# Optimization experiments

Hardware: AMD Instinct MI355X
Metric: run time of the kernel (lower is better)

## Reference

```python
import jax, jax.numpy as jnp
import numpy as np

C = 256        # in_channels == depth
HEADS = 8
K = 251        # kernel_size == attended axis length
DH = C // HEADS  # 32
EPS = 1e-5


def _bn(x, g, b, axes, ch_axis):
    # training-mode batchnorm: batch statistics, biased variance
    m = jnp.mean(x, axes, keepdims=True)
    v = jnp.var(x, axes, keepdims=True)
    shape = [1] * x.ndim
    shape[ch_axis] = -1
    return (x - m) / jnp.sqrt(v + EPS) * g.reshape(shape) + b.reshape(shape)


def _axial_cross(x, y, wk, wq, wv, gk, bk, gq, bq, gkq, bkq, glog, blog, rel):
    B, _, H, W = x.shape  # [B, C, H, W], height_dim=False -> attend over W
    # permute(0,2,1,3) then fold freq axis into batch: [B*H, C, W]
    xb = x.transpose(0, 2, 1, 3).reshape(B * H, C, W)
    yb = y.transpose(0, 2, 1, 3).reshape(B * H, C, W)
    # 1x1 conv1d == channel-mixing einsum, then BN over (batch, length)
    k = _bn(jnp.einsum('oc,bcl->bol', wk, xb), gk, bk, (0, 2), 1)
    q = _bn(jnp.einsum('oc,bcl->bol', wq, yb), gq, bq, (0, 2), 1)
    v = _bn(jnp.einsum('oc,bcl->bol', wv, xb), gkq, bkq, (0, 2), 1)  # original uses kq_bn on v
    kqv = jnp.concatenate([k, q, v], axis=1).reshape(B * H, HEADS, DH * 2, W)
    k = kqv[:, :, : DH // 2]          # [b, h, dh/2, W]
    q = kqv[:, :, DH // 2: DH]        # [b, h, dh/2, W]
    v = kqv[:, :, DH:]                # [b, h, dh,   W]
    # relative position encodings gathered by distance
    ki = jnp.arange(K)
    dist = (ki[None, :] - ki[:, None] + K - 1).reshape(-1)
    rel_e = rel[:, dist].reshape(DH * 2, K, K)
    q_enc = rel_e[: DH // 2]
    k_enc = rel_e[DH // 2: DH]
    v_enc = rel_e[DH:]
    qk = jnp.einsum('bhdx,bhdy->bhxy', q, k)
    qr = jnp.einsum('bhdx,dxy->bhxy', q, q_enc)
    kr = jnp.einsum('bhdx,dxy->bhxy', k, k_enc).transpose(0, 1, 3, 2)
    logits = jnp.concatenate([qk, qr, kr], axis=1)  # [b, 3*h, W, W]
    logits = _bn(logits, glog, blog, (0, 2, 3), 1)  # BatchNorm2d on 3*h channels
    logits = logits.reshape(B * H, 3, HEADS, W, W).sum(axis=1)
    weights = jax.nn.softmax(logits, axis=3)
    attn = jnp.einsum('bhxy,bhdy->bhdx', weights, v)        # [b, h, dh, W]
    attn_enc = jnp.einsum('bhxy,dxy->bhdx', weights, v_enc)  # [b, h, dh, W]
    attn_out = jnp.concatenate([attn, attn_enc], axis=-1)    # cat along length axis (as in original)
    attn_out = attn_out.reshape(B * H, C * 2, W)
    out = attn_out.reshape(B, H, C, 2, W).sum(axis=3)        # [B, H, C, W]
    return out.transpose(0, 2, 1, 3)                          # [B, C, H, W]


def setup_inputs() -> dict:
    key = jax.random.key(0)
    ks = jax.random.split(key, 6)
    B, H, W = 2, 15, 251
    sc = 0.05
    return {
        'x': jax.random.normal(ks[0], (B, C, H, W), jnp.float32),
        'y': jax.random.normal(ks[1], (B, C, H, W), jnp.float32),
        'wk': jax.random.normal(ks[2], (C // 2, C), jnp.float32) * sc,
        'wq': jax.random.normal(ks[3], (C // 2, C), jnp.float32) * sc,
        'wv': jax.random.normal(ks[4], (C, C), jnp.float32) * sc,
        'gk': jnp.ones((C // 2,), jnp.float32), 'bk': jnp.zeros((C // 2,), jnp.float32),
        'gq': jnp.ones((C // 2,), jnp.float32), 'bq': jnp.zeros((C // 2,), jnp.float32),
        'gkq': jnp.ones((C,), jnp.float32), 'bkq': jnp.zeros((C,), jnp.float32),
        'glog': jnp.ones((HEADS * 3,), jnp.float32), 'blog': jnp.zeros((HEADS * 3,), jnp.float32),
        'rel': jax.random.normal(ks[5], (DH * 2, 2 * K - 1), jnp.float32),
    }


def reference(x, y, wk, wq, wv, gk, bk, gq, bq, gkq, bkq, glog, blog, rel):
    return _axial_cross(x, y, wk, wq, wv, gk, bk, gq, bq, gkq, bkq, glog, blog, rel)
```

## Files before the change

### kernel.cpp

```cpp
#include <hip/hip_runtime.h>
#include <hip/hip_bf16.h>
#include <cstdint>

#define WPOS 251
#define NBB  30
#define NCH  512
#define RELP 501
#define NEPS 1e-5f

typedef _Float16 half2_t __attribute__((ext_vector_type(2)));
typedef _Float16 half8_t __attribute__((ext_vector_type(8)));
typedef float f32x16_t __attribute__((ext_vector_type(16)));

#if defined(__has_builtin)
#if __has_builtin(__builtin_amdgcn_fdot2)
#define FDOT2(a, b, c) __builtin_amdgcn_fdot2((a), (b), (c), false)
#endif
#endif
#ifndef FDOT2
#define FDOT2(a, b, c) ((float)(a)[0] * (float)(b)[0] + (float)(a)[1] * (float)(b)[1] + (c))
#endif

static constexpr size_t SZ_Z     = (size_t)NBB * NCH * WPOS;
static constexpr size_t OFF_Z    = 0;
static constexpr size_t OFF_VH   = OFF_Z + SZ_Z;
static constexpr size_t SZ_VH    = (size_t)NBB * 8 * 128 * 32;
static constexpr size_t OFF_RETC = OFF_VH + SZ_VH;
static constexpr size_t OFF_VETP = OFF_RETC + (size_t)RELP * 16;
static constexpr size_t OFF_P1Q  = OFF_VETP + (size_t)256 * 32;
static constexpr size_t OFF_P1K  = OFF_P1Q + (size_t)16 * 502;
static constexpr size_t OFF_P2Q  = OFF_P1K + (size_t)16 * 502;
static constexpr size_t OFF_P2K  = OFF_P2Q + (size_t)256 * 502;
static constexpr size_t OFF_LPP  = OFF_P2K + (size_t)256 * 502;
static constexpr size_t OFF_CPS  = OFF_LPP + (size_t)960 * 548;
static constexpr size_t OFF_CPS2 = OFF_CPS + (size_t)240 * 512;
static constexpr size_t OFF_CS   = OFF_CPS2 + (size_t)240 * 512;
static constexpr size_t OFF_CS2  = OFF_CS + 512;
static constexpr size_t OFF_LPF  = OFF_CS2 + 512;

static __device__ __forceinline__ unsigned packh2(float a, float b) {
  half2_t t;
  t[0] = (_Float16)a;
  t[1] = (_Float16)b;
  return __builtin_bit_cast(unsigned, t);
}
static __device__ __forceinline__ half2_t ash2(unsigned u) {
  return __builtin_bit_cast(half2_t, u);
}

__global__ __launch_bounds__(256) void k_pre(
    const float* __restrict__ rel, unsigned* __restrict__ retc, unsigned* __restrict__ vetp,
    float* __restrict__ p1q, float* __restrict__ p1k,
    float* __restrict__ p2q, float* __restrict__ p2k) {
  int blk = blockIdx.x;
  if (blk < 64) {
    int idx = blk * 256 + threadIdx.x;
    if (idx < RELP * 16) {
      int p = idx >> 4, j = idx & 15;
      float lo, hi;
      if (j < 8) {
        lo = rel[(size_t)(2 * j) * RELP + p];
        hi = rel[(size_t)(2 * j + 1) * RELP + p];
      } else {
        int jj = j - 8;
        lo = rel[(size_t)(16 + 2 * jj) * RELP + (500 - p)];
        hi = rel[(size_t)(17 + 2 * jj) * RELP + (500 - p)];
      }
      retc[(size_t)p * 16 + j] = packh2(lo, hi);
    } else if (idx < RELP * 16 + 256 * 32) {
      int i2 = idx - RELP * 16;
      int t = i2 >> 5, ch = i2 & 31;
      float lo = (2 * t <= 500) ? rel[(size_t)(32 + ch) * RELP + 2 * t] : 0.f;
      float hi = (2 * t + 1 <= 500) ? rel[(size_t)(32 + ch) * RELP + 2 * t + 1] : 0.f;
      vetp[(size_t)t * 32 + ch] = packh2(lo, hi);
    }
    return;
  }
  int task = blk - 64;
  const float* ra;
  const float* rb = nullptr;
  float* outp;
  if (task < 16)        { ra = rel + (size_t)task * RELP; outp = p1q + (size_t)task * 502; }
  else if (task < 32)   { ra = rel + (size_t)task * RELP; outp = p1k + (size_t)(task - 16) * 502; }
  else if (task < 288)  { int pr = task - 32;
                          ra = rel + (size_t)(pr >> 4) * RELP;
                          rb = rel + (size_t)(pr & 15) * RELP;
                          outp = p2q + (size_t)pr * 502; }
  else                  { int pr = task - 288;
                          ra = rel + (size_t)(16 + (pr >> 4)) * RELP;
                          rb = rel + (size_t)(16 + (pr & 15)) * RELP;
                          outp = p2k + (size_t)pr * 502; }
  __shared__ float buf[256];
  int t = threadIdx.x;
  int i0 = 2 * t, i1 = 2 * t + 1;
  float a0 = (i0 < RELP) ? (rb ? ra[i0] * rb[i0] : ra[i0]) : 0.f;
  float a1 = (i1 < RELP) ? (rb ? ra[i1] * rb[i1] : ra[i1]) : 0.f;
  buf[t] = a0 + a1;
  __syncthreads();
#pragma unroll
  for (int off = 1; off < 256; off <<= 1) {
    float v = buf[t];
    float add = (t >= off) ? buf[t - off] : 0.f;
    __syncthreads();
    buf[t] = v + add;
    __syncthreads();
  }
  float ex = buf[t] - (a0 + a1);
  if (i0 <= RELP) outp[i0] = ex;
  if (i1 <= RELP) outp[i1] = ex + a0;
}

__global__ __launch_bounds__(256) void k_gemm(
    const float* __restrict__ x, const float* __restrict__ y,
    const float* __restrict__ wk, const float* __restrict__ wq,
    const float* __restrict__ wv, float* __restrict__ z,
    float* __restrict__ cps, float* __restrict__ cps2) {
  int l0 = blockIdx.x * 64;
  int o0 = blockIdx.y * 64;
  int bb = blockIdx.z;
  int b = bb / 15, hi = bb % 15;
  const float* src;
  const float* wmat;
  int orow0;
  if (o0 < 128)      { wmat = wk; orow0 = o0;       src = x; }
  else if (o0 < 256) { wmat = wq; orow0 = o0 - 128; src = y; }
  else               { wmat = wv; orow0 = o0 - 256; src = x; }

  __shared__ _Float16 Ah[64][68];
  __shared__ _Float16 Bh[64][68];

  int tid = threadIdx.x;
  int lane = tid & 63, wv4 = tid >> 6;
  int wo = wv4 >> 1, wl = wv4 & 1;
  int m = lane & 31, kh = lane >> 5;

  f32x16_t acc = {};

  int cA = tid & 63, ogA = tid >> 6;
  int lB = tid & 63, kgB = tid >> 6;
  int lglob = l0 + lB;
  bool lok = (lglob < WPOS);
  const float* xcol = src + (size_t)(((size_t)b * 256) * 15 + hi) * WPOS + lglob;

  for (int c0 = 0; c0 < 256; c0 += 64) {
#pragma unroll
    for (int i = 0; i < 16; ++i) {
      int o = ogA * 16 + i;
      Ah[o][cA] = (_Float16)wmat[(size_t)(orow0 + o) * 256 + c0 + cA];
    }
#pragma unroll
    for (int i = 0; i < 16; ++i) {
      int k = kgB * 16 + i;
      float v = lok ? xcol[(size_t)(c0 + k) * 15 * WPOS] : 0.f;
      Bh[k][lB] = (_Float16)v;
    }
    __syncthreads();
#pragma unroll
    for (int ks = 0; ks < 4; ++ks) {
      const _Float16* ap = &Ah[wo * 32 + m][ks * 16 + kh * 8];
      uint2 aLo = *(const uint2*)(ap);
      uint2 aHi = *(const uint2*)(ap + 4);
      uint4 au = {aLo.x, aLo.y, aHi.x, aHi.y};
      half8_t af = __builtin_bit_cast(half8_t, au);
      half8_t bf;
      int kb = ks * 16 + kh * 8;
      int bcol = wl * 32 + m;
#pragma unroll
      for (int e = 0; e < 8; ++e) bf[e] = Bh[kb + e][bcol];
      acc = __builtin_amdgcn_mfma_f32_32x32x16_f16(af, bf, acc, 0, 0, 0);
    }
    __syncthreads();
  }

  int n = lane & 31;
  int lout = l0 + wl * 32 + n;
  if (lout < WPOS) {
#pragma unroll
    for (int r = 0; r < 16; ++r) {
      int mrow = (r & 3) + 8 * (r >> 2) + 4 * kh;
      int o = o0 + wo * 32 + mrow;
      z[((size_t)bb * NCH + o) * WPOS + lout] = acc[r];
    }
  }

  int part = (blockIdx.x * 2 + wl) * NBB + bb;
#pragma unroll
  for (int r = 0; r < 16; ++r) {
    float s = acc[r];
    float s2 = s * s;
#pragma unroll
    for (int m2 = 1; m2 < 32; m2 <<= 1) {
      s  += __shfl_xor(s, m2, 64);
      s2 += __shfl_xor(s2, m2, 64);
    }
    if (n == 0) {
      int mrow = (r & 3) + 8 * (r >> 2) + 4 * kh;
      int o = o0 + wo * 32 + mrow;
      cps[(size_t)part * 512 + o] = s;
      cps2[(size_t)part * 512 + o] = s2;
    }
  }
}

__global__ __launch_bounds__(256) void k_cred(
    const float* __restrict__ cps, const float* __restrict__ cps2,
    float* __restrict__ csum, float* __restrict__ csum2) {
  int c = blockIdx.x * 16 + (threadIdx.x & 15);
  int grp = threadIdx.x >> 4;
  __shared__ float r1[256], r2[256];
  float s = 0.f, s2 = 0.f;
  for (int i = 0; i < 15; ++i) {
    int p = grp * 15 + i;
    s += cps[(size_t)p * 512 + c];
    s2 += cps2[(size_t)p * 512 + c];
  }
  r1[threadIdx.x] = s; r2[threadIdx.x] = s2;
  __syncthreads();
  for (int st = 128; st >= 16; st >>= 1) {
    if (threadIdx.x < st) {
      r1[threadIdx.x] += r1[threadIdx.x + st];
      r2[threadIdx.x] += r2[threadIdx.x + st];
    }
    __syncthreads();
  }
  if (threadIdx.x < 16) {
    csum[c] = r1[threadIdx.x];
    csum2[c] = r2[threadIdx.x];
  }
}

__device__ __forceinline__ float block_reduce(float v, float* red, int tid) {
  red[tid] = v; __syncthreads();
  for (int s = 128; s > 0; s >>= 1) {
    if (tid < s) red[tid] += red[tid + s];
    __syncthreads();
  }
  float r = red[0]; __syncthreads();
  return r;
}

__device__ __forceinline__ void chan_affine(
    int ch, const float* gk, const float* bk, const float* gq, const float* bq,
    const float* gkq, const float* bkq, const float* csum, const float* csum2,
    float& a, float& bout) {
  float g, bi;
  if (ch < 128)      { g = gk[ch];        bi = bk[ch]; }
  else if (ch < 256) { g = gq[ch - 128];  bi = bq[ch - 128]; }
  else               { g = gkq[ch - 256]; bi = bkq[ch - 256]; }
  float n = (float)(NBB * WPOS);
  float mean = csum[ch] / n;
  float var = csum2[ch] / n - mean * mean;
  a = g / sqrtf(var + NEPS);
  bout = bi - mean * a;
}

__global__ __launch_bounds__(256) void k_mid(
    const float* __restrict__ z,
    const float* __restrict__ gk, const float* __restrict__ bk,
    const float* __restrict__ gq, const float* __restrict__ bq,
    const float* __restrict__ gkq, const float* __restrict__ bkq,
    const float* __restrict__ csum, const float* __restrict__ csum2,
    unsigned* __restrict__ vh,
    const float* __restrict__ p1q, const float* __restrict__ p1k,
    const float* __restrict__ p2q, const float* __restrict__ p2k,
    float* __restrict__ lpp) {
  int blk = blockIdx.x;
  bool isV = (blk < 960);
  int sblk = isV ? blk : blk - 960;
  int bbh = sblk % 240, sub = sblk / 240;
  int bb = bbh >> 3, h = bbh & 7;
  int tid = threadIdx.x;

  __shared__ __align__(16) float pool[16 * 68 * 2];
  __shared__ float red[256];
  __shared__ float caL[32], cbL[32];
  __shared__ int pairLUT[136];

  if (tid < 32) {
    int ch = h * 64 + (isV ? 32 + tid : tid);
    chan_affine(ch, gk, bk, gq, bq, gkq, bkq, csum, csum2, caL[tid], cbL[tid]);
  } else if (tid >= 64 && tid < 200) {
    int i = tid - 64, rem = i, d = 0;
    while (rem >= 16 - d) { rem -= 16 - d; ++d; }
    pairLUT[i] = (d << 4) | (d + rem);
  }
  __syncthreads();

  if (isV) {
    float (*T)[65] = (float(*)[65])pool;
    int l0 = sub * 64;
    const float* zv = z + ((size_t)bb * NCH + h * 64 + 32) * WPOS;
    for (int i = tid; i < 32 * 64; i += 256) {
      int ch = i >> 6, l = i & 63;
      int gl = l0 + l;
      T[ch][l] = (gl < WPOS) ? (caL[ch] * zv[(size_t)ch * WPOS + gl] + cbL[ch]) : 0.f;
    }
    __syncthreads();
    int p0 = l0 >> 1;
    for (int i = tid; i < 32 * 32; i += 256) {
      int pl = i >> 5, ch = i & 31;
      int gp = p0 + pl;
      if (gp < 128)
        vh[((size_t)bbh * 128 + gp) * 32 + ch] = packh2(T[ch][2 * pl], T[ch][2 * pl + 1]);
    }
    return;
  }

  float (*qs)[68] = (float(*)[68])pool;
  float (*ks)[68] = (float(*)[68])(pool + 16 * 68);
  int x0 = sub * 64;
  const float* zb = z + ((size_t)bb * NCH + h * 64) * WPOS;
  for (int idx = tid; idx < 16 * 64; idx += 256) {
    int d = idx >> 6, xl = idx & 63;
    int xg = x0 + xl;
    float kv = 0.f, qv = 0.f;
    if (xg < WPOS) {
      kv = caL[d] * zb[(size_t)d * WPOS + xg] + cbL[d];
      qv = caL[16 + d] * zb[(size_t)(16 + d) * WPOS + xg] + cbL[16 + d];
    }
    ks[d][xl] = kv; qs[d][xl] = qv;
  }
  __syncthreads();
  float* outp = lpp + ((size_t)bbh * 4 + sub) * 548;
  if (tid < 16) {
    float s = 0.f;
    for (int xl = 0; xl < 64; ++xl) s += qs[tid][xl];
    outp[516 + tid] = s;
  } else if (tid < 32) {
    float s = 0.f;
    for (int xl = 0; xl < 64; ++xl) s += ks[tid - 16][xl];
    outp[532 + (tid - 16)] = s;
  }
  {
    int d = tid >> 4, d2 = tid & 15;
    float g1 = 0.f, g2 = 0.f;
    for (int xl = 0; xl < 64; ++xl) {
      g1 += qs[d][xl] * qs[d2][xl];
      g2 += ks[d][xl] * ks[d2][xl];
    }
    outp[tid] = g1;
    outp[256 + tid] = g2;
  }
  float v_sumqr = 0.f, v_sqqr = 0.f, v_sumkr = 0.f, v_sqkr = 0.f;
  {
    int xl = tid & 63, wv = tid >> 6;
    int xg = x0 + xl;
    if (xg < WPOS) {
      int ihi = 501 - xg, ilo = 250 - xg;
      for (int i = wv; i < 136; i += 4) {
        int pc = pairLUT[i];
        int d = pc >> 4, d2 = pc & 15;
        float wgt = (d == d2) ? 1.f : 2.f;
        const float* pq = p2q + (size_t)(d * 16 + d2) * 502;
        const float* pk = p2k + (size_t)(d * 16 + d2) * 502;
        v_sqqr += wgt * qs[d][xl] * qs[d2][xl] * (pq[ihi] - pq[ilo]);
        v_sqkr += wgt * ks[d][xl] * ks[d2][xl] * (pk[ihi] - pk[ilo]);
      }
      for (int d = wv; d < 16; d += 4) {
        v_sumqr += qs[d][xl] * (p1q[d * 502 + ihi] - p1q[d * 502 + ilo]);
        v_sumkr += ks[d][xl] * (p1k[d * 502 + ihi] - p1k[d * 502 + ilo]);
      }
    }
  }
  float r1 = block_reduce(v_sumqr, red, tid);
  float r2 = block_reduce(v_sqqr, red, tid);
  float r3 = block_reduce(v_sumkr, red, tid);
  float r4 = block_reduce(v_sqkr, red, tid);
  if (tid == 0) { outp[512] = r1; outp[513] = r2; outp[514] = r3; outp[515] = r4; }
}

__global__ __launch_bounds__(256) void k_lstats2(const float* __restrict__ lpp,
                                                 float* __restrict__ lp) {
  int bbh = blockIdx.x;
  int tid = threadIdx.x;
  __shared__ float red[256];
  __shared__ float qsums[16], ksums[16];
  const float* b0 = lpp + (size_t)bbh * 4 * 548;
  float qg = b0[tid] + b0[548 + tid] + b0[1096 + tid] + b0[1644 + tid];
  float kg = b0[256 + tid] + b0[804 + tid] + b0[1352 + tid] + b0[1900 + tid];
  if (tid < 16) {
    qsums[tid] = b0[516 + tid] + b0[1064 + tid] + b0[1612 + tid] + b0[2160 + tid];
    ksums[tid] = b0[532 + tid] + b0[1080 + tid] + b0[1628 + tid] + b0[2176 + tid];
  }
  float sqqk = block_reduce(qg * kg, red, tid);
  if (tid == 0) {
    float sum_qk = 0.f;
    for (int d = 0; d < 16; ++d) sum_qk += qsums[d] * ksums[d];
    float s1 = 0.f, s2 = 0.f, s3 = 0.f, s4 = 0.f;
    for (int c = 0; c < 4; ++c) {
      const float* bc = b0 + (size_t)c * 548;
      s1 += bc[512]; s2 += bc[513]; s3 += bc[514]; s4 += bc[515];
    }
    float* o = lp + (size_t)bbh * 6;
    o[0] = sum_qk; o[1] = sqqk;
    o[2] = s1; o[3] = s2; o[4] = s3; o[5] = s4;
  }
}

__global__ __launch_bounds__(256) void k_attn(
    const float* __restrict__ z,
    const float* __restrict__ gk, const float* __restrict__ bk,
    const float* __restrict__ gq, const float* __restrict__ bq,
    const float* __restrict__ gkq, const float* __restrict__ bkq,
    const float* __restrict__ csum, const float* __restrict__ csum2,
    const unsigned* __restrict__ vh,
    const unsigned* __restrict__ retc, const unsigned* __restrict__ vetp,
    const float* __restrict__ lp, const float* __restrict__ glog,
    float* __restrict__ out) {
  int blk = blockIdx.x;
  int bbh = blk % 240, tile = blk / 240;
  int bb = bbh >> 3, h = bbh & 7;
  int b = bb / 15, hi = bb % 15;
  int x0 = tile * 32;
  int nr = min(32, WPOS - x0);
  int tid = threadIdx.x;
  int lane = tid & 63, wvid = tid >> 6;

  const float LOG2E = 1.4426950408889634f;

  __shared__ __align__(16) unsigned Su[32 * 132];
  __shared__ __align__(16) unsigned winU[282 * 18];
  __shared__ __align__(16) unsigned uSh[256];
  __shared__ float affL[72];
  _Float16* S = (_Float16*)Su;
  unsigned* qsP = uSh;
  float* sred = (float*)uSh;
  float* Cred = (float*)winU;

  int pwin0 = 251 - x0 - nr;
  int nwin = 250 + nr;

  if (tid < 32) {
    int ch = h * 64 + tid;
    chan_affine(ch, gk, bk, gq, bq, gkq, bkq, csum, csum2, affL[tid], affL[32 + tid]);
  } else if (tid >= 64 && tid < 70) {
    int grp = (tid - 64) >> 1, off = (tid - 64) & 1;
    float s = 0.f;
    for (int bb2 = 0; bb2 < NBB; ++bb2)
      s += lp[(size_t)(bb2 * 8 + h) * 6 + grp * 2 + off];
    affL[64 + (tid - 64)] = s;
  }
  __syncthreads();
  float la_qk, la_qr, la_kr;
  {
    float n = (float)NBB * (float)WPOS * (float)WPOS;
    float m0 = affL[64] / n, v0 = affL[65] / n - m0 * m0;
    float m1 = affL[66] / n, v1 = affL[67] / n - m1 * m1;
    float m2 = affL[68] / n, v2 = affL[69] / n - m2 * m2;
    la_qk = glog[0 * 8 + h] / sqrtf(v0 + NEPS) * LOG2E;
    la_qr = glog[1 * 8 + h] / sqrtf(v1 + NEPS) * LOG2E;
    la_kr = glog[2 * 8 + h] / sqrtf(v2 + NEPS) * LOG2E;
  }

  const float* zb = z + ((size_t)bb * NCH + h * 64) * WPOS;

  for (int i = tid; i < nwin * 16; i += 256) {
    int r = i >> 4, j = i & 15;
    winU[r * 18 + j] = retc[(size_t)(pwin0 + r) * 16 + j];
  }

  {
    int xx = tid & 31, j = tid >> 5;
    int xcl = min(x0 + xx, WPOS - 1);
    float q0 = affL[16 + 2 * j] * zb[(size_t)(16 + 2 * j) * WPOS + xcl] + affL[48 + 2 * j];
    float q1 = affL[17 + 2 * j] * zb[(size_t)(17 + 2 * j) * WPOS + xcl] + affL[49 + 2 * j];
    qsP[xx * 8 + j] = packh2(q0, q1);
  }

  int yy = wvid * 64 + lane;
  int yc = min(yy, WPOS - 1);
  bool yok = (yy < WPOS);
  half2_t khv[8];
#pragma unroll
  for (int d = 0; d < 8; ++d) {
    float k0 = affL[2 * d]     * zb[(size_t)(2 * d) * WPOS + yc] + affL[32 + 2 * d];
    float k1 = affL[2 * d + 1] * zb[(size_t)(2 * d + 1) * WPOS + yc] + affL[33 + 2 * d];
    khv[d] = __builtin_bit_cast(half2_t, packh2(k0, k1));
  }
  __syncthreads();

  {
    int rowbase = yc + nr - 1;
    for (int xx = 0; xx < nr; ++xx) {
      const unsigned* wr = &winU[(size_t)(rowbase - xx) * 18];
      const unsigned* qp = &qsP[xx * 8];
      float dqk = 0.f, dqr = 0.f, dkr = 0.f;
#pragma unroll
      for (int j2 = 0; j2 < 4; ++j2) {
        uint2 ue = *(const uint2*)(wr + 2 * j2);
        uint2 uk = *(const uint2*)(wr + 8 + 2 * j2);
        uint2 uq = *(const uint2*)(qp + 2 * j2);
        half2_t qe0 = ash2(ue.x), qe1 = ash2(ue.y);
        half2_t ke0 = ash2(uk.x), ke1 = ash2(uk.y);
        half2_t q0  = ash2(uq.x), q1  = ash2(uq.y);
        half2_t k0 = khv[2 * j2], k1 = khv[2 * j2 + 1];
        dqk = FDOT2(q0, k0, dqk);  dqk = FDOT2(q1, k1, dqk);
        dqr = FDOT2(q0, qe0, dqr); dqr = FDOT2(q1, qe1, dqr);
        dkr = FDOT2(k0, ke0, dkr); dkr = FDOT2(k1, ke1, dkr);
      }
      float sval = la_qk * dqk + la_qr * dqr + la_kr * dkr;
      S[xx * 264 + yy] = yok ? (_Float16)sval : (_Float16)0.f;
    }
  }
  for (int i = tid; i < 32 * 8; i += 256)
    S[(i >> 3) * 264 + 256 + (i & 7)] = (_Float16)0.f;
  if (nr < 32) {
    int ntail = (32 - nr) * 264;
    for (int i = tid; i < ntail; i += 256) S[nr * 264 + i] = (_Float16)0.f;
  }
  __syncthreads();

  int xx = lane & 31;
  int sl = wvid * 2 + (lane >> 5);
  int ylo = sl * 32;
  const unsigned* Srp = Su + xx * 132;
  {
    float m = -1e30f;
    if (sl < 7) {
#pragma unroll
      for (int pp = 0; pp < 16; ++pp) {
        half2_t hp = ash2(Srp[(ylo >> 1) + pp]);
        m = fmaxf(m, fmaxf((float)hp[0], (float)hp[1]));
      }
    } else {
#pragma unroll
      for (int pp = 0; pp < 13; ++pp) {
        half2_t hp = ash2(Srp[112 + pp]);
        m = fmaxf(m, fmaxf((float)hp[0], (float)hp[1]));
      }
      m = fmaxf(m, (float)S[xx * 264 + 250]);
    }
    sred[sl * 32 + xx] = m;
  }
  __syncthreads();
  float rowm = sred[0 * 32 + xx];
#pragma unroll
  for (int s = 1; s < 8; ++s) rowm = fmaxf(rowm, sred[s * 32 + xx]);
  __syncthreads();
  {
    float sacc = 0.f;
    unsigned* Swp = Su + xx * 132;
    if (sl < 7) {
#pragma unroll
      for (int pp = 0; pp < 16; ++pp) {
        half2_t hp = ash2(Swp[(ylo >> 1) + pp]);
        float e0 = exp2f((float)hp[0] - rowm);
        float e1 = exp2f((float)hp[1] - rowm);
        Swp[(ylo >> 1) + pp] = packh2(e0, e1);
        sacc += e0 + e1;
      }
    } else {
#pragma unroll
      for (int pp = 0; pp < 13; ++pp) {
        half2_t hp = ash2(Swp[112 + pp]);
        float e0 = exp2f((float)hp[0] - rowm);
        float e1 = exp2f((float)hp[1] - rowm);
        Swp[112 + pp] = packh2(e0, e1);
        sacc += e0 + e1;
      }
      float e = exp2f((float)S[xx * 264 + 250] - rowm);
      S[xx * 264 + 250] = (_Float16)e;
      sacc += e;
    }
    sred[sl * 32 + xx] = sacc;
  }
  __syncthreads();
  float denom = 0.f;
#pragma unroll
  for (int s = 0; s < 8; ++s) denom += sred[s * 32 + xx];

  f32x16_t acc = {};
  int xcol = lane & 31;
  int khh = lane >> 5;
  const _Float16* Srow = S + xcol * 264;
  {
    const unsigned* vhb = vh + (size_t)bbh * 128 * 32 + xcol;
#pragma unroll
    for (int ks = 0; ks < 4; ++ks) {
      int y0 = 64 * wvid + 16 * ks + 8 * khh;
      int t0 = y0 >> 1;
      uint4 au = {vhb[(size_t)(t0 + 0) * 32], vhb[(size_t)(t0 + 1) * 32],
                  vhb[(size_t)(t0 + 2) * 32], vhb[(size_t)(t0 + 3) * 32]};
      half8_t af = __builtin_bit_cast(half8_t, au);
      half8_t bf = *(const half8_t*)(Srow + y0);
      acc = __builtin_amdgcn_mfma_f32_32x32x16_f16(af, bf, acc, 0, 0, 0);
    }
    const unsigned* vpb = vetp + xcol;
    int ybase = xcol + x0 - 250;
#pragma unroll
    for (int ks = 0; ks < 8; ++ks) {
      int p0 = 128 * wvid + 16 * ks + 8 * khh;
      int t0 = p0 >> 1;
      uint4 au = {vpb[(size_t)(t0 + 0) * 32], vpb[(size_t)(t0 + 1) * 32],
                  vpb[(size_t)(t0 + 2) * 32], vpb[(size_t)(t0 + 3) * 32]};
      half8_t af = __builtin_bit_cast(half8_t, au);
      half8_t bf;
#pragma unroll
      for (int e = 0; e < 8; ++e) {
        int yv = ybase + p0 + e;
        bf[e] = ((unsigned)yv < 264u) ? Srow[yv] : (_Float16)0.f;
      }
      acc = __builtin_amdgcn_mfma_f32_32x32x16_f16(af, bf, acc, 0, 0, 0);
    }
  }

  if (wvid > 0) {
    float* cp = Cred + ((size_t)(wvid - 1) * 64 + lane) * 17;
#pragma unroll
    for (int r = 0; r < 16; ++r) cp[r] = acc[r];
  }
  __syncthreads();
  if (wvid == 0) {
#pragma unroll
    for (int w2 = 0; w2 < 3; ++w2) {
      const float* cp = Cred + ((size_t)w2 * 64 + lane) * 17;
#pragma unroll
      for (int r = 0; r < 16; ++r) acc[r] += cp[r];
    }
    if (xcol < nr) {
      float rinv = 1.0f / denom;
      int xg = x0 + xcol;
#pragma unroll
      for (int r = 0; r < 16; ++r) {
        int d = (r & 3) + 8 * (r >> 2) + 4 * khh;
        out[(((size_t)b * 256 + h * 32 + d) * 15 + hi) * WPOS + xg] = acc[r] * rinv;
      }
    }
  }
}

extern "C" void kernel_launch(void* const* d_in, const int* in_sizes, int n_in,
                              void* d_out, int out_size, void* d_ws, size_t ws_size,
                              hipStream_t stream) {
  const float* x    = (const float*)d_in[0];
  const float* y    = (const float*)d_in[1];
  const float* wk   = (const float*)d_in[2];
  const float* wq   = (const float*)d_in[3];
  const float* wv   = (const float*)d_in[4];
  const float* gk   = (const float*)d_in[5];
  const float* bk   = (const float*)d_in[6];
  const float* gq   = (const float*)d_in[7];
  const float* bq   = (const float*)d_in[8];
  const float* gkq  = (const float*)d_in[9];
  const float* bkq  = (const float*)d_in[10];
  const float* glog = (const float*)d_in[11];
  const float* rel  = (const float*)d_in[13];
  float* out = (float*)d_out;
  float* ws  = (float*)d_ws;

  float* z      = ws + OFF_Z;
  unsigned* vh  = (unsigned*)(ws + OFF_VH);
  unsigned* retc= (unsigned*)(ws + OFF_RETC);
  unsigned* vetp= (unsigned*)(ws + OFF_VETP);
  float* p1q    = ws + OFF_P1Q;
  float* p1k    = ws + OFF_P1K;
  float* p2q    = ws + OFF_P2Q;
  float* p2k    = ws + OFF_P2K;
  float* lpp    = ws + OFF_LPP;
  float* cps    = ws + OFF_CPS;
  float* cps2   = ws + OFF_CPS2;
  float* csum   = ws + OFF_CS;
  float* csum2  = ws + OFF_CS2;
  float* lp     = ws + OFF_LPF;

  k_pre<<<608, 256, 0, stream>>>(rel, retc, vetp, p1q, p1k, p2q, p2k);
  dim3 g1(4, 8, NBB);
  k_gemm<<<g1, 256, 0, stream>>>(x, y, wk, wq, wv, z, cps, cps2);
  k_cred<<<32, 256, 0, stream>>>(cps, cps2, csum, csum2);
  k_mid<<<1920, 256, 0, stream>>>(z, gk, bk, gq, bq, gkq, bkq, csum, csum2,
                                  vh, p1q, p1k, p2q, p2k, lpp);
  k_lstats2<<<240, 256, 0, stream>>>(lpp, lp);
  k_attn<<<240 * 8, 256, 0, stream>>>(z, gk, bk, gq, bq, gkq, bkq, csum, csum2,
                                      vh, retc, vetp, lp, glog, out);
}
```

Before: 107.9 us.

## Fuse rel-table precompute into GEMM launch and precompute windowed prefix differences

```diff
diff --git a/kernel.cpp b/kernel.cpp
--- a/kernel.cpp
+++ b/kernel.cpp
@@ -27,11 +27,11 @@
 static constexpr size_t SZ_VH    = (size_t)NBB * 8 * 128 * 32;
 static constexpr size_t OFF_RETC = OFF_VH + SZ_VH;
 static constexpr size_t OFF_VETP = OFF_RETC + (size_t)RELP * 16;
-static constexpr size_t OFF_P1Q  = OFF_VETP + (size_t)256 * 32;
-static constexpr size_t OFF_P1K  = OFF_P1Q + (size_t)16 * 502;
-static constexpr size_t OFF_P2Q  = OFF_P1K + (size_t)16 * 502;
-static constexpr size_t OFF_P2K  = OFF_P2Q + (size_t)256 * 502;
-static constexpr size_t OFF_LPP  = OFF_P2K + (size_t)256 * 502;
+static constexpr size_t OFF_D1Q  = OFF_VETP + (size_t)256 * 32;
+static constexpr size_t OFF_D1K  = OFF_D1Q + (size_t)16 * 256;
+static constexpr size_t OFF_D2Q  = OFF_D1K + (size_t)16 * 256;
+static constexpr size_t OFF_D2K  = OFF_D2Q + (size_t)136 * 256;
+static constexpr size_t OFF_LPP  = OFF_D2K + (size_t)136 * 256;
 static constexpr size_t OFF_CPS  = OFF_LPP + (size_t)960 * 548;
 static constexpr size_t OFF_CPS2 = OFF_CPS + (size_t)240 * 512;
 static constexpr size_t OFF_CS   = OFF_CPS2 + (size_t)240 * 512;
@@ -48,13 +48,19 @@
   return __builtin_bit_cast(half2_t, u);
 }
 
-__global__ __launch_bounds__(256) void k_pre(
-    const float* __restrict__ rel, unsigned* __restrict__ retc, unsigned* __restrict__ vetp,
-    float* __restrict__ p1q, float* __restrict__ p1k,
-    float* __restrict__ p2q, float* __restrict__ p2k) {
+__global__ __launch_bounds__(256) void k_gemm_pre(
+    const float* __restrict__ x, const float* __restrict__ y,
+    const float* __restrict__ wk, const float* __restrict__ wq,
+    const float* __restrict__ wv, const float* __restrict__ rel,
+    float* __restrict__ z, float* __restrict__ cps, float* __restrict__ cps2,
+    unsigned* __restrict__ retc, unsigned* __restrict__ vetp,
+    float* __restrict__ d1q, float* __restrict__ d1k,
+    float* __restrict__ d2q, float* __restrict__ d2k) {
   int blk = blockIdx.x;
+  int tid = threadIdx.x;
+
   if (blk < 64) {
-    int idx = blk * 256 + threadIdx.x;
+    int idx = blk * 256 + tid;
     if (idx < RELP * 16) {
       int p = idx >> 4, j = idx & 15;
       float lo, hi;
@@ -76,48 +82,55 @@
     }
     return;
   }
-  int task = blk - 64;
-  const float* ra;
-  const float* rb = nullptr;
-  float* outp;
-  if (task < 16)        { ra = rel + (size_t)task * RELP; outp = p1q + (size_t)task * 502; }
-  else if (task < 32)   { ra = rel + (size_t)task * RELP; outp = p1k + (size_t)(task - 16) * 502; }
-  else if (task < 288)  { int pr = task - 32;
-                          ra = rel + (size_t)(pr >> 4) * RELP;
-                          rb = rel + (size_t)(pr & 15) * RELP;
-                          outp = p2q + (size_t)pr * 502; }
-  else                  { int pr = task - 288;
-                          ra = rel + (size_t)(16 + (pr >> 4)) * RELP;
-                          rb = rel + (size_t)(16 + (pr & 15)) * RELP;
-                          outp = p2k + (size_t)pr * 502; }
-  __shared__ float buf[256];
-  int t = threadIdx.x;
-  int i0 = 2 * t, i1 = 2 * t + 1;
-  float a0 = (i0 < RELP) ? (rb ? ra[i0] * rb[i0] : ra[i0]) : 0.f;
-  float a1 = (i1 < RELP) ? (rb ? ra[i1] * rb[i1] : ra[i1]) : 0.f;
-  buf[t] = a0 + a1;
-  __syncthreads();
-#pragma unroll
-  for (int off = 1; off < 256; off <<= 1) {
-    float v = buf[t];
-    float add = (t >= off) ? buf[t - off] : 0.f;
+
+  if (blk < 368) {
+    int task = blk - 64;
+    const float* ra;
+    const float* rb = nullptr;
+    float* outD;
+    if (task < 16)      { ra = rel + (size_t)task * RELP; outD = d1q + (size_t)task * 256; }
+    else if (task < 32) { ra = rel + (size_t)task * RELP; outD = d1k + (size_t)(task - 16) * 256; }
+    else {
+      int i = (task < 168) ? task - 32 : task - 168;
+      int rem = i, d = 0;
+      while (rem >= 16 - d) { rem -= 16 - d; ++d; }
+      int d2 = d + rem;
+      if (task < 168) {
+        ra = rel + (size_t)d * RELP; rb = rel + (size_t)d2 * RELP;
+        outD = d2q + (size_t)i * 256;
+      } else {
+        ra = rel + (size_t)(16 + d) * RELP; rb = rel + (size_t)(16 + d2) * RELP;
+        outD = d2k + (size_t)i * 256;
+      }
+    }
+    __shared__ float buf[256];
+    __shared__ float pbuf[502];
+    int t = tid;
+    int i0 = 2 * t, i1 = 2 * t + 1;
+    float a0 = (i0 < RELP) ? (rb ? ra[i0] * rb[i0] : ra[i0]) : 0.f;
+    float a1 = (i1 < RELP) ? (rb ? ra[i1] * rb[i1] : ra[i1]) : 0.f;
+    buf[t] = a0 + a1;
     __syncthreads();
-    buf[t] = v + add;
+#pragma unroll
+    for (int off = 1; off < 256; off <<= 1) {
+      float v = buf[t];
+      float add = (t >= off) ? buf[t - off] : 0.f;
+      __syncthreads();
+      buf[t] = v + add;
+      __syncthreads();
+    }
+    float ex = buf[t] - (a0 + a1);
+    if (i0 <= RELP) pbuf[i0] = ex;
+    if (i1 <= RELP) pbuf[i1] = ex + a0;
     __syncthreads();
-  }
-  float ex = buf[t] - (a0 + a1);
-  if (i0 <= RELP) outp[i0] = ex;
-  if (i1 <= RELP) outp[i1] = ex + a0;
-}
-
-__global__ __launch_bounds__(256) void k_gemm(
-    const float* __restrict__ x, const float* __restrict__ y,
-    const float* __restrict__ wk, const float* __restrict__ wq,
-    const float* __restrict__ wv, float* __restrict__ z,
-    float* __restrict__ cps, float* __restrict__ cps2) {
-  int l0 = blockIdx.x * 64;
-  int o0 = blockIdx.y * 64;
-  int bb = blockIdx.z;
+    if (t <= 250) outD[t] = pbuf[501 - t] - pbuf[250 - t];
+    return;
+  }
+
+  int g = blk - 368;
+  int l0 = (g & 3) * 64;
+  int o0 = ((g >> 2) & 7) * 64;
+  int bb = g >> 5;
   int b = bb / 15, hi = bb % 15;
   const float* src;
   const float* wmat;
@@ -129,7 +142,6 @@
   __shared__ _Float16 Ah[64][68];
   __shared__ _Float16 Bh[64][68];
 
-  int tid = threadIdx.x;
   int lane = tid & 63, wv4 = tid >> 6;
   int wo = wv4 >> 1, wl = wv4 & 1;
   int m = lane & 31, kh = lane >> 5;
@@ -183,7 +195,7 @@
     }
   }
 
-  int part = (blockIdx.x * 2 + wl) * NBB + bb;
+  int part = ((g & 3) * 2 + wl) * NBB + bb;
 #pragma unroll
   for (int r = 0; r < 16; ++r) {
     float s = acc[r];
@@ -261,8 +273,8 @@
     const float* __restrict__ gkq, const float* __restrict__ bkq,
     const float* __restrict__ csum, const float* __restrict__ csum2,
     unsigned* __restrict__ vh,
-    const float* __restrict__ p1q, const float* __restrict__ p1k,
-    const float* __restrict__ p2q, const float* __restrict__ p2k,
+    const float* __restrict__ d1q, const float* __restrict__ d1k,
+    const float* __restrict__ d2q, const float* __restrict__ d2k,
     float* __restrict__ lpp) {
   int blk = blockIdx.x;
   bool isV = (blk < 960);
@@ -346,19 +358,16 @@
     int xl = tid & 63, wv = tid >> 6;
     int xg = x0 + xl;
     if (xg < WPOS) {
-      int ihi = 501 - xg, ilo = 250 - xg;
       for (int i = wv; i < 136; i += 4) {
         int pc = pairLUT[i];
         int d = pc >> 4, d2 = pc & 15;
         float wgt = (d == d2) ? 1.f : 2.f;
-        const float* pq = p2q + (size_t)(d * 16 + d2) * 502;
-        const float* pk = p2k + (size_t)(d * 16 + d2) * 502;
-        v_sqqr += wgt * qs[d][xl] * qs[d2][xl] * (pq[ihi] - pq[ilo]);
-        v_sqkr += wgt * ks[d][xl] * ks[d2][xl] * (pk[ihi] - pk[ilo]);
+        v_sqqr += wgt * qs[d][xl] * qs[d2][xl] * d2q[(size_t)i * 256 + xg];
+        v_sqkr += wgt * ks[d][xl] * ks[d2][xl] * d2k[(size_t)i * 256 + xg];
       }
       for (int d = wv; d < 16; d += 4) {
-        v_sumqr += qs[d][xl] * (p1q[d * 502 + ihi] - p1q[d * 502 + ilo]);
-        v_sumkr += ks[d][xl] * (p1k[d * 502 + ihi] - p1k[d * 502 + ilo]);
+        v_sumqr += qs[d][xl] * d1q[(size_t)d * 256 + xg];
+        v_sumkr += ks[d][xl] * d1k[(size_t)d * 256 + xg];
       }
     }
   }
@@ -652,10 +661,10 @@
   unsigned* vh  = (unsigned*)(ws + OFF_VH);
   unsigned* retc= (unsigned*)(ws + OFF_RETC);
   unsigned* vetp= (unsigned*)(ws + OFF_VETP);
-  float* p1q    = ws + OFF_P1Q;
-  float* p1k    = ws + OFF_P1K;
-  float* p2q    = ws + OFF_P2Q;
-  float* p2k    = ws + OFF_P2K;
+  float* d1q    = ws + OFF_D1Q;
+  float* d1k    = ws + OFF_D1K;
+  float* d2q    = ws + OFF_D2Q;
+  float* d2k    = ws + OFF_D2K;
   float* lpp    = ws + OFF_LPP;
   float* cps    = ws + OFF_CPS;
   float* cps2   = ws + OFF_CPS2;
@@ -663,12 +672,11 @@
   float* csum2  = ws + OFF_CS2;
   float* lp     = ws + OFF_LPF;
 
-  k_pre<<<608, 256, 0, stream>>>(rel, retc, vetp, p1q, p1k, p2q, p2k);
-  dim3 g1(4, 8, NBB);
-  k_gemm<<<g1, 256, 0, stream>>>(x, y, wk, wq, wv, z, cps, cps2);
+  k_gemm_pre<<<1328, 256, 0, stream>>>(x, y, wk, wq, wv, rel, z, cps, cps2,
+                                       retc, vetp, d1q, d1k, d2q, d2k);
   k_cred<<<32, 256, 0, stream>>>(cps, cps2, csum, csum2);
   k_mid<<<1920, 256, 0, stream>>>(z, gk, bk, gq, bq, gkq, bkq, csum, csum2,
-                                  vh, p1q, p1k, p2q, p2k, lpp);
+                                  vh, d1q, d1k, d2q, d2k, lpp);
   k_lstats2<<<240, 256, 0, stream>>>(lpp, lp);
   k_attn<<<240 * 8, 256, 0, stream>>>(z, gk, bk, gq, bq, gkq, bkq, csum, csum2,
                                       vh, retc, vetp, lp, glog, out);
```

New measurement: 100.7 us. 6.6% less time.
